# Performance work log

Measured on AMD Instinct MI355X. Metric: run time of the kernel, lower is better.

## Reference

```python
import jax, jax.numpy as jnp
import numpy as np

THETA = 10.0      # spike threshold
TAU_SR = 10.0     # synaptic (PSP) alpha-kernel time constant
TAU_REF = 1.0     # refractory alpha-kernel time constant
SCALE_REF = 2.0   # refractory scale (kernel = -scaleRef*theta*(t/tauRef)e^{1-t/tauRef})
TAU_RHO = 1.0     # surrogate-gradient width
SCALE_RHO = 1.0   # surrogate-gradient scale
TS = 1.0          # simulation step (ms)
E = 2.718281828459045

@jax.custom_vjp
def spike_surrogate(u):
    return (u >= THETA).astype(u.dtype)

def _spike_fwd(u):
    return (u >= THETA).astype(u.dtype), u

def _spike_bwd(u, g):
    # SLAYER surrogate spike-pdf gradient
    pdf = (SCALE_RHO / TAU_RHO) * jnp.exp(-jnp.abs(u - THETA) / TAU_RHO)
    return (g * pdf,)

spike_surrogate.defvjp(_spike_fwd, _spike_bwd)

def psp_spike(x):
    # x: (N, ..., T). PSP = causal temporal conv with alpha kernel
    # eps(t) = (t/tauSr) e^{1-t/tauSr}, realized EXACTLY as a 2-state IIR recursion.
    # spike = threshold; each emitted spike injects refractory alpha kernel
    # -scaleRef*theta*(t/tauRef) e^{1-t/tauRef} into the future membrane.
    xt = jnp.moveaxis(x, -1, 0)  # (T, ...)
    a_sr = jnp.exp(jnp.asarray(-TS / TAU_SR, x.dtype))
    a_rf = jnp.exp(jnp.asarray(-TS / TAU_REF, x.dtype))
    c_sr = E / TAU_SR
    c_rf = -SCALE_REF * THETA * E / TAU_REF
    z = jnp.zeros_like(xt[0])
    def step(carry, xi):
        gp, hp, gr, hr = carry
        hp = a_sr * (hp + gp)
        gp = a_sr * gp + xi
        hr = a_rf * (hr + gr)   # same recursion over past spikes
        gr = a_rf * gr
        u = c_sr * hp + c_rf * hr  # membrane = PSP + refractory
        s = spike_surrogate(u)
        return (gp, hp, gr + s, hr), s
    _, st = jax.lax.scan(step, (z, z, z, z), xt)
    return jnp.moveaxis(st, 0, -1)

def sum_pool(x, k):
    # SLAYER pool: conv with constant weight 1.1*theta over kxk window, stride k
    N, C, H, W, T = x.shape
    xs = x.reshape(N, C, H // k, k, W // k, k, T).sum(axis=(3, 5))
    return 1.1 * THETA * xs

def conv2dt(x, w, pad):
    # SLAYER conv = conv3d with kernel (k,k,1): per-time-step 2D conv, T as trailing dim
    return jax.lax.conv_general_dilated(
        x, w[..., None], (1, 1, 1),
        [(pad, pad), (pad, pad), (0, 0)],
        dimension_numbers=('NCHWT', 'OIHWT', 'NCHWT'))

def forward(s_in, w1, w2, w3, w4a, w4b):
    x = psp_spike(sum_pool(s_in, 4))              # (N,2,32,32,T)
    x = psp_spike(conv2dt(x, w1, 2))              # (N,32,32,32,T)
    x = psp_spike(sum_pool(x, 2))                 # (N,32,16,16,T)
    x = psp_spike(conv2dt(x, w2, 1))              # (N,64,16,16,T)
    x = psp_spike(sum_pool(x, 2))                 # (N,64,8,8,T)
    x = psp_spike(conv2dt(x, w3, 1))              # (N,64,8,8,T)
    N, T = x.shape[0], x.shape[-1]
    xf = x.reshape(N, -1, T)                      # (N, 64*8*8, T)
    x = psp_spike(jnp.einsum('nft,of->not', xf, w4a))  # (N,256,T)
    x = psp_spike(jnp.einsum('nct,oc->not', x, w4b))   # (N,11,T)
    return x

def setup_inputs():
    key = jax.random.key(0)
    ks = jax.random.split(key, 6)
    N, T = 4, 300
    # Bernoulli(0.05) event spikes, DVS128 gesture format (N,2,128,128,T)
    s_in = (jax.random.uniform(ks[0], (N, 2, 128, 128, T)) < 0.05).astype(jnp.float32)
    w1 = jax.random.normal(ks[1], (32, 2, 5, 5), jnp.float32) * 10.0 * 0.05   # weightScale=10
    w2 = jax.random.normal(ks[2], (64, 32, 3, 3), jnp.float32) * 20.0 * 0.01  # weightScale=20
    w3 = jax.random.normal(ks[3], (64, 64, 3, 3), jnp.float32) * 20.0 * 0.01  # weightScale=20
    w4a = jax.random.normal(ks[4], (256, 64 * 8 * 8), jnp.float32) * 0.01
    w4b = jax.random.normal(ks[5], (11, 256), jnp.float32) * 0.05
    return {"s_in": s_in, "w1": w1, "w2": w2, "w3": w3, "w4a": w4a, "w4b": w4b}

def reference(s_in, w1, w2, w3, w4a, w4b):
    return forward(s_in, w1, w2, w3, w4a, w4b)
```

## Files before the change

### kernel.cpp

```cpp
#include <hip/hip_runtime.h>
#include <cstdint>

#define TT 300
#define TC 75
#define NBATCH 4

typedef float pf2 __attribute__((ext_vector_type(2)));
typedef _Float16 h8t __attribute__((ext_vector_type(8)));
typedef float f32x4 __attribute__((ext_vector_type(4)));

__device__ __forceinline__ void psp_step(float z, float& gp, float& hp, float& gr, float& hr, float& s_out) {
    hp = 0.90483741803595957f * (hp + gp);
    gp = 0.90483741803595957f * gp + z;
    hr = 0.36787944117144233f * (hr + gr);
    gr = 0.36787944117144233f * gr;
    float u = 0.27182818284590452f * hp + (-54.365636569180904f) * hr;
    float s = (u >= 10.0f) ? 1.0f : 0.0f;
    gr += s;
    s_out = s;
}

template <int R>
__global__ void k_scan_redp(const float* __restrict__ z, float* __restrict__ s,
                            int n_neur, int pstride) {
    int i = blockIdx.x * 64 + threadIdx.x;
    if (i >= n_neur) return;
    const float* zp = z + (size_t)i * TT;
    float* sp = s + (size_t)i * TT;
    float gp = 0.f, hp = 0.f, gr = 0.f, hr = 0.f;
#pragma unroll 1
    for (int c = 0; c < 25; ++c) {
        const float* p = zp + c * 12;
        float4 a0 = *(const float4*)(p);
        float4 a1 = *(const float4*)(p + 4);
        float4 a2 = *(const float4*)(p + 8);
#pragma unroll
        for (int r = 1; r < R; ++r) {
            const float* pr = p + (size_t)r * pstride;
            float4 b0 = *(const float4*)(pr);
            float4 b1 = *(const float4*)(pr + 4);
            float4 b2 = *(const float4*)(pr + 8);
            a0.x += b0.x; a0.y += b0.y; a0.z += b0.z; a0.w += b0.w;
            a1.x += b1.x; a1.y += b1.y; a1.z += b1.z; a1.w += b1.w;
            a2.x += b2.x; a2.y += b2.y; a2.z += b2.z; a2.w += b2.w;
        }
        float4 o0, o1, o2;
        psp_step(a0.x, gp, hp, gr, hr, o0.x);
        psp_step(a0.y, gp, hp, gr, hr, o0.y);
        psp_step(a0.z, gp, hp, gr, hr, o0.z);
        psp_step(a0.w, gp, hp, gr, hr, o0.w);
        psp_step(a1.x, gp, hp, gr, hr, o1.x);
        psp_step(a1.y, gp, hp, gr, hr, o1.y);
        psp_step(a1.z, gp, hp, gr, hr, o1.z);
        psp_step(a1.w, gp, hp, gr, hr, o1.w);
        psp_step(a2.x, gp, hp, gr, hr, o2.x);
        psp_step(a2.y, gp, hp, gr, hr, o2.y);
        psp_step(a2.z, gp, hp, gr, hr, o2.z);
        psp_step(a2.w, gp, hp, gr, hr, o2.w);
        float* q = sp + c * 12;
        *(float4*)(q) = o0;
        *(float4*)(q + 4) = o1;
        *(float4*)(q + 8) = o2;
    }
}

__global__ void k_scan16_f16(const float* __restrict__ z, _Float16* __restrict__ s16) {
    int i = blockIdx.x * 64 + threadIdx.x;
    int n = i >> 12, f = i & 4095;
    const float* zp = z + (size_t)i * 16;
    _Float16* sp = s16 + ((size_t)n * TT) * 4096 + f;
    float gp = 0.f, hp = 0.f, gr = 0.f, hr = 0.f;
#define SC16_CHUNK(TCI, NTT) do {                                              \
    const float* pp = zp + (size_t)(TCI) * (16384 * 16);                       \
    float4 a0 = *(const float4*)(pp);                                          \
    float4 a1 = *(const float4*)(pp + 4);                                      \
    float4 a2 = *(const float4*)(pp + 8);                                      \
    float4 a3 = *(const float4*)(pp + 12);                                     \
    float zv[16] = {a0.x,a0.y,a0.z,a0.w,a1.x,a1.y,a1.z,a1.w,                   \
                    a2.x,a2.y,a2.z,a2.w,a3.x,a3.y,a3.z,a3.w};                  \
    _Pragma("unroll")                                                          \
    for (int tt = 0; tt < (NTT); ++tt) {                                       \
        float o;                                                               \
        psp_step(zv[tt], gp, hp, gr, hr, o);                                   \
        sp[(size_t)((TCI) * 16 + tt) * 4096] = (_Float16)o;                    \
    }                                                                          \
} while (0)
#pragma unroll 1
    for (int tcc = 0; tcc < 18; ++tcc) SC16_CHUNK(tcc, 16);
    SC16_CHUNK(18, 12);
#undef SC16_CHUNK
}

template <int C, int H2, int W2>
__global__ void __launch_bounds__(256) k_spsq16(const float* __restrict__ z,
                                                _Float16* __restrict__ s16) {
    constexpr int H = 2 * H2, W = 2 * W2;
    constexpr int NP = NBATCH * C * H * W;
    constexpr int C8 = C / 8;
    __shared__ _Float16 tile[16 * C];

    int i = blockIdx.x * 256 + threadIdx.x;
    int q = i & 3;
    int p = i >> 2;
    int c  = p % C;
    int x2 = (p / C) % W2;
    int y2 = (p / (C * W2)) % H2;
    int n  = p / (C * W2 * H2);
    int dy = q >> 1, dx = q & 1;
    int pz = ((n * C + c) * H + 2 * y2 + dy) * W + 2 * x2 + dx;
    const float* zp = z + (size_t)pz * 16;

    int tid = threadIdx.x;
    int wt  = tid & 15;
    int wc8 = tid >> 4;
    int p0 = blockIdx.x * 64;
    int wx2 = (p0 / C) % W2;
    int wy2 = (p0 / (C * W2)) % H2;
    int wn  = p0 / (C * W2 * H2);
    _Float16* wbase = s16 + ((((size_t)(wn * C8 + wc8) * H2 + wy2) * W2 + wx2) * TT) * 8;

    float gp = 0.f, hp = 0.f, gr = 0.f, hr = 0.f;
    float Gp = 0.f, Hp = 0.f, Gr = 0.f, Hr = 0.f;
#define SPSQ_CHUNK(TCI, NTT) do {                                              \
    const float* pp = zp + (size_t)(TCI) * (NP * 16);                          \
    float4 a0 = *(const float4*)(pp);                                          \
    float4 a1 = *(const float4*)(pp + 4);                                      \
    float4 a2 = *(const float4*)(pp + 8);                                      \
    float4 a3 = *(const float4*)(pp + 12);                                     \
    float zv[16] = {a0.x,a0.y,a0.z,a0.w,a1.x,a1.y,a1.z,a1.w,                   \
                    a2.x,a2.y,a2.z,a2.w,a3.x,a3.y,a3.z,a3.w};                  \
    float ov[16];                                                              \
    _Pragma("unroll")                                                          \
    for (int tt = 0; tt < (NTT); ++tt) {                                       \
        float sq;                                                              \
        psp_step(zv[tt], gp, hp, gr, hr, sq);                                  \
        float t1 = sq + __shfl_xor(sq, 1, 64);                                 \
        float pool = t1 + __shfl_xor(t1, 2, 64);                               \
        psp_step(11.0f * pool, Gp, Hp, Gr, Hr, ov[tt]);                        \
    }                                                                          \
    __syncthreads();                                                           \
    if (q == 0) {                                                              \
        _Pragma("unroll")                                                      \
        for (int tt = 0; tt < (NTT); ++tt)                                     \
            tile[tt * C + c] = (_Float16)ov[tt];                               \
    }                                                                          \
    __syncthreads();                                                           \
    if (tid < 16 * C8 && wt < (NTT)) {                                         \
        h8t v = *(const h8t*)(tile + wt * C + wc8 * 8);                        \
        *(h8t*)(wbase + (size_t)((TCI) * 16 + wt) * 8) = v;                    \
    }                                                                          \
} while (0)
#pragma unroll 1
    for (int tcc = 0; tcc < 18; ++tcc) SPSQ_CHUNK(tcc, 16);
    SPSQ_CHUNK(18, 12);
#undef SPSQ_CHUNK
}

__global__ void k_pack_wmfma(const float* __restrict__ w, _Float16* __restrict__ wm,
                             int CIN, int COUT, int total) {
    int i = blockIdx.x * 256 + threadIdx.x;
    if (i >= total) return;
    int lane = i & 63;
    int r = i >> 6;
    int ver = r & 1; r >>= 1;
    int KC = CIN >> 5, CT = COUT >> 4;
    int ct = r % CT; r /= CT;
    int kc = r % KC;
    int tap = r / KC;
    int ky = tap / 3, kx = tap % 3;
    int co  = ct * 16 + (lane & 15);
    int ci0 = kc * 32 + (lane >> 4) * 8;
    _Float16 out[8];
#pragma unroll
    for (int j = 0; j < 8; ++j) {
        float wf = w[((co * CIN + ci0 + j) * 3 + ky) * 3 + kx];
        _Float16 hi = (_Float16)wf;
        out[j] = ver ? (_Float16)((wf - (float)hi) * 4096.0f) : hi;
    }
    *(h8t*)(wm + (size_t)i * 8) = *(h8t*)out;
}

__global__ void k_pack_wfc(const float* __restrict__ w, _Float16* __restrict__ wm,
                           int FIN, int COUT, int total) {
    int i = blockIdx.x * 256 + threadIdx.x;
    if (i >= total) return;
    int lane = i & 63;
    int r = i >> 6;
    int ver = r & 1; r >>= 1;
    int CT = COUT >> 4;
    int ct = r % CT;
    int kg = r / CT;
    int co = ct * 16 + (lane & 15);
    int f0 = kg * 32 + (lane >> 4) * 8;
    _Float16 out[8];
#pragma unroll
    for (int j = 0; j < 8; ++j) {
        float wf = w[(size_t)co * FIN + f0 + j];
        _Float16 hi = (_Float16)wf;
        out[j] = ver ? (_Float16)((wf - (float)hi) * 4096.0f) : hi;
    }
    *(h8t*)(wm + (size_t)i * 8) = *(h8t*)out;
}

__global__ void k_pack_wl1(const float* __restrict__ w, _Float16* __restrict__ wm) {
    int i = blockIdx.x * 256 + threadIdx.x;
    if (i >= 768) return;
    int lane = i & 63;
    int r = i >> 6;
    int ver = r & 1;
    int ch = (r >> 1) & 1;
    int kc = r >> 2;
    int co = ch * 16 + (lane & 15);
    int k0 = kc * 32 + (lane >> 4) * 8;
    _Float16 out[8];
#pragma unroll
    for (int j = 0; j < 8; ++j) {
        int k = k0 + j;
        int ky = k >> 4, slot = k & 15, kx = slot >> 1, ci = slot & 1;
        float wf = (ky < 5 && kx < 5) ? w[((co * 2 + ci) * 5 + ky) * 5 + kx] : 0.f;
        _Float16 hif = (_Float16)wf;
        out[j] = ver ? (_Float16)((wf - (float)hif) * 4096.0f) : hif;
    }
    *(h8t*)(wm + (size_t)i * 8) = *(h8t*)out;
}

__global__ void k_pool4(const float* __restrict__ x, float* __restrict__ z) {
    int idx = blockIdx.x * 256 + threadIdx.x;
    if (idx >= NBATCH * 2 * 32 * 32 * TC) return;
    int tc = idx % TC;
    int p  = idx / TC;
    int w  = p % 32;
    int h  = (p / 32) % 32;
    int nc = p / (32 * 32);
    const float* base = x + (((size_t)nc * 128 + h * 4) * 128 + w * 4) * TT + tc * 4;
    float ax = 0.f, ay = 0.f, az = 0.f, aw = 0.f;
#pragma unroll
    for (int i = 0; i < 4; ++i)
#pragma unroll
        for (int j = 0; j < 4; ++j) {
            float4 v = *(const float4*)(base + ((size_t)i * 128 + j) * TT);
            ax += v.x; ay += v.y; az += v.z; aw += v.w;
        }
    float4 o; o.x = 11.0f * ax; o.y = 11.0f * ay; o.z = 11.0f * az; o.w = 11.0f * aw;
    *(float4*)(z + (size_t)p * TT + tc * 4) = o;
}

__global__ void __launch_bounds__(256) k_l1_fused(const float* __restrict__ s0,
                                                  const _Float16* __restrict__ wl1,
                                                  _Float16* __restrict__ s2h) {
    constexpr int NT = 19;
    __shared__ _Float16 stage[7 * 16 * 40];
    __shared__ float    trans[256 * 17];
    __shared__ _Float16 tile[4 * 16 * 16];

    int bid = blockIdx.x;
    int y2 = bid & 15;
    int xh = (bid >> 4) & 3;
    int ch = (bid >> 6) & 1;
    int n  = bid >> 7;
    int tid = threadIdx.x;
    int lane = tid & 63;
    int wv = tid >> 6;
    int tl = lane & 15;
    int hi = lane >> 4;
    int yy = wv >> 1;
    int xq = wv & 1;

    int q    = tid & 3;
    int co_s = (tid >> 2) & 15;
    int x2l_s = tid >> 6;
    int wt  = tid & 15;
    int wc8 = (tid >> 4) & 1;
    int wx  = tid >> 5;

    const h8t* wv4 = (const h8t*)wl1;
    float gp = 0.f, hp = 0.f, gr = 0.f, hr = 0.f;
    float Gp = 0.f, Hp = 0.f, Gr = 0.f, Hr = 0.f;

#pragma unroll 1
    for (int tc = 0; tc < NT; ++tc) {
        __syncthreads();
#pragma unroll
        for (int ii = 0; ii < 14; ++ii) {
            int i = tid + ii * 256;
            int t  = i & 15;
            int lx = (i >> 4) & 15;
            int ci = (i >> 8) & 1;
            int r  = i >> 9;
            int gx = xh * 8 + lx - 2;
            int yi = y2 * 2 + r - 2;
            int tg = tc * 16 + t;
            float v = 0.f;
            if (gx >= 0 && gx < 32 && yi >= 0 && yi < 32 && tg < TT)
                v = s0[(((size_t)(n * 2 + ci) * 32 + yi) * 32 + gx) * TT + tg];
            stage[(r * 16 + t) * 40 + lx * 2 + ci] = (_Float16)v;
        }
        __syncthreads();
        f32x4 ah4[4], al4[4];
#pragma unroll
        for (int xi = 0; xi < 4; ++xi) { ah4[xi] = (f32x4){0.f,0.f,0.f,0.f}; al4[xi] = (f32x4){0.f,0.f,0.f,0.f}; }
#pragma unroll
        for (int kc = 0; kc < 3; ++kc) {
            h8t wa = wv4[((kc * 2 + ch) * 2 + 0) * 64 + lane];
            h8t wb = wv4[((kc * 2 + ch) * 2 + 1) * 64 + lane];
            int row = yy + 2 * kc + (hi >> 1);
#pragma unroll
            for (int xi = 0; xi < 4; ++xi) {
                int xo = xq * 4 + xi;
                const uint32_t* lp = (const uint32_t*)(stage + (row * 16 + tl) * 40 + xo * 2 + (hi & 1) * 8);
                union { uint32_t u[4]; h8t h; } bu;
                bu.u[0] = lp[0]; bu.u[1] = lp[1]; bu.u[2] = lp[2]; bu.u[3] = lp[3];
                ah4[xi] = __builtin_amdgcn_mfma_f32_16x16x32_f16(wa, bu.h, ah4[xi], 0, 0, 0);
                al4[xi] = __builtin_amdgcn_mfma_f32_16x16x32_f16(wb, bu.h, al4[xi], 0, 0, 0);
            }
        }
#pragma unroll
        for (int xi = 0; xi < 4; ++xi) {
            int xo = xq * 4 + xi;
#pragma unroll
            for (int r = 0; r < 4; ++r) {
                float u = ah4[xi][r] + al4[xi][r] * 2.44140625e-4f;
                int rowt = ((xo >> 1) * 16 + hi * 4 + r) * 4 + yy * 2 + (xo & 1);
                trans[rowt * 17 + tl] = u;
            }
        }
        __syncthreads();
#pragma unroll
        for (int t = 0; t < 16; ++t) {
            float u = trans[tid * 17 + t];
            float sq;
            psp_step(u, gp, hp, gr, hr, sq);
            float t1 = sq + __shfl_xor(sq, 1, 64);
            float pool = t1 + __shfl_xor(t1, 2, 64);
            float ov;
            psp_step(11.0f * pool, Gp, Hp, Gr, Hr, ov);
            if (q == 0) tile[(x2l_s * 16 + t) * 16 + co_s] = (_Float16)ov;
        }
        __syncthreads();
        if (tid < 128) {
            int tg = tc * 16 + wt;
            if (tg < TT) {
                h8t v = *(const h8t*)(tile + (wx * 16 + wt) * 16 + wc8 * 8);
                int cg8 = ch * 2 + wc8;
                int x2g = xh * 4 + wx;
                *(h8t*)(s2h + ((((size_t)(n * 4 + cg8) * 16 + y2) * 16 + x2g) * (size_t)TT + tg) * 8) = v;
            }
        }
    }
}

template <int CIN, int COUT, int H, int W, int YPB>
__global__ void __launch_bounds__(256, 2) k_conv_mfma(const _Float16* __restrict__ s16,
                                                      const _Float16* __restrict__ wm,
                                                      float* __restrict__ z) {
    constexpr int NT = 19;
    constexpr int KC = CIN / 32;
    constexpr int CH = CIN / 8;
    constexpr int XL = W + 2;
    constexpr int CT = COUT / 16;
    constexpr int XPW = W / 4;
    constexpr int ROWS = YPB + 2;
    constexpr int NP = NBATCH * COUT * H * W;
    __shared__ _Float16 lds[ROWS * XL * 16 * CIN];

    int bid = blockIdx.x;
    int tc = bid % NT;
    int yb = ((bid / NT) % (H / YPB)) * YPB;
    int n  = bid / (NT * (H / YPB));
    int tid = threadIdx.x;

    constexpr int TOT = ROWS * XL * CH * 16;
    for (int i = tid; i < TOT; i += 256) {
        int t   = i & 15;
        int c   = (i >> 4) % CH;
        int xc  = ((i >> 4) / CH) % XL;
        int row = ((i >> 4) / CH) / XL;
        int tg = tc * 16 + t;
        int xi = xc - 1;
        int yi = yb + row - 1;
        h8t v;
#pragma unroll
        for (int e = 0; e < 8; ++e) v[e] = (_Float16)0.0f;
        if (xi >= 0 && xi < W && yi >= 0 && yi < H && tg < TT)
            v = *(const h8t*)(s16 + ((((size_t)(n * CH + c) * H + yi) * W + xi) * TT + tg) * 8);
        int swz = (CIN == 32) ? ((t >> 1) & 3) : (t & 7);
        int off = ((row * XL + xc) * 16 + t) * CIN + ((c ^ swz) << 3);
        *(h8t*)(lds + off) = v;
    }
    __syncthreads();

    int lane = tid & 63;
    int wv   = tid >> 6;
    int tl   = lane & 15;
    int hi   = lane >> 4;
    const h8t* wmv = (const h8t*)wm;
    int swz = (CIN == 32) ? ((tl >> 1) & 3) : (tl & 7);

#pragma unroll
    for (int yy = 0; yy < YPB; ++yy) {
        f32x4 acc_h[XPW][CT], acc_l[XPW][CT];
#pragma unroll
        for (int a = 0; a < XPW; ++a)
#pragma unroll
            for (int b = 0; b < CT; ++b) {
                acc_h[a][b] = (f32x4){0.f, 0.f, 0.f, 0.f};
                acc_l[a][b] = (f32x4){0.f, 0.f, 0.f, 0.f};
            }
#pragma unroll
        for (int ky = 0; ky < 3; ++ky) {
#pragma unroll
            for (int kx = 0; kx < 3; ++kx) {
                int tap = ky * 3 + kx;
#pragma unroll
                for (int kc = 0; kc < KC; ++kc) {
                    h8t bf[XPW];
#pragma unroll
                    for (int xi = 0; xi < XPW; ++xi) {
                        int x = wv * XPW + xi;
                        int c = kc * 4 + hi;
                        int off = (((yy + ky) * XL + (x + kx)) * 16 + tl) * CIN + ((c ^ swz) << 3);
                        bf[xi] = *(const h8t*)(lds + off);
                    }
#pragma unroll
                    for (int ct = 0; ct < CT; ++ct) {
                        size_t wbase = ((size_t)(tap * KC + kc) * CT + ct) * 2;
                        h8t ah = wmv[(wbase + 0) * 64 + lane];
                        h8t al = wmv[(wbase + 1) * 64 + lane];
#pragma unroll
                        for (int xi = 0; xi < XPW; ++xi) {
                            acc_h[xi][ct] = __builtin_amdgcn_mfma_f32_16x16x32_f16(ah, bf[xi], acc_h[xi][ct], 0, 0, 0);
                            acc_l[xi][ct] = __builtin_amdgcn_mfma_f32_16x16x32_f16(al, bf[xi], acc_l[xi][ct], 0, 0, 0);
                        }
                    }
                }
            }
        }
#pragma unroll
        for (int xi = 0; xi < XPW; ++xi) {
            int x = wv * XPW + xi;
#pragma unroll
            for (int ct = 0; ct < CT; ++ct) {
#pragma unroll
                for (int r = 0; r < 4; ++r) {
                    int co = ct * 16 + hi * 4 + r;
                    int pz = ((n * COUT + co) * H + (yb + yy)) * W + x;
                    z[((size_t)tc * NP + pz) * 16 + tl]
                        = acc_h[xi][ct][r] + acc_l[xi][ct][r] * 2.44140625e-4f;
                }
            }
        }
    }
}

template <int FIN, int OUT>
__global__ void __launch_bounds__(256) k_fc_mfma(const _Float16* __restrict__ s16,
                                                 const _Float16* __restrict__ wm,
                                                 float* __restrict__ z) {
    constexpr int NT = 19;
    constexpr int CT = OUT / 16;
    constexpr int KCH = 512;
    constexpr int NK = FIN / KCH;
    __shared__ _Float16 lds[KCH * 16];

    int bid = blockIdx.x;
    int tc = bid % NT;
    int n  = (bid / NT) % NBATCH;
    int cg = bid / (NT * NBATCH);
    int tid = threadIdx.x;
    int lane = tid & 63, wv = tid >> 6;
    int tl = lane & 15, hi = lane >> 4;
    int ct = cg * 4 + wv;

    f32x4 acc_h = (f32x4){0.f, 0.f, 0.f, 0.f};
    f32x4 acc_l = (f32x4){0.f, 0.f, 0.f, 0.f};
    const h8t* wmv = (const h8t*)wm;

    for (int kb = 0; kb < NK; ++kb) {
        __syncthreads();
#pragma unroll
        for (int j = 0; j < 4; ++j) {
            int chunk = tid + j * 256;
            int c = chunk & 63;
            int t = chunk >> 6;
            int tg = tc * 16 + t;
            h8t v;
#pragma unroll
            for (int e = 0; e < 8; ++e) v[e] = (_Float16)0.0f;
            if (tg < TT) v = *(const h8t*)(s16 + ((size_t)(n * TT + tg) * FIN + kb * KCH + c * 8));
            *(h8t*)(lds + ((t * 64 + (c ^ (t & 7))) << 3)) = v;
        }
        __syncthreads();
#pragma unroll
        for (int kc = 0; kc < KCH / 32; ++kc) {
            int c = kc * 4 + hi;
            h8t bf = *(const h8t*)(lds + ((tl * 64 + (c ^ (tl & 7))) << 3));
            size_t wbase = ((size_t)((kb * (KCH / 32) + kc) * CT + ct)) * 2;
            h8t ah = wmv[(wbase + 0) * 64 + lane];
            h8t al = wmv[(wbase + 1) * 64 + lane];
            acc_h = __builtin_amdgcn_mfma_f32_16x16x32_f16(ah, bf, acc_h, 0, 0, 0);
            acc_l = __builtin_amdgcn_mfma_f32_16x16x32_f16(al, bf, acc_l, 0, 0, 0);
        }
    }
    int tg = tc * 16 + tl;
    if (tg < TT) {
#pragma unroll
        for (int r = 0; r < 4; ++r) {
            int co = ct * 16 + hi * 4 + r;
            z[(size_t)(n * OUT + co) * TT + tg] = acc_h[r] + acc_l[r] * 2.44140625e-4f;
        }
    }
}

template <int OUT, int FIN, int OPER, int FSPLIT>
__global__ void k_fc_a(const float* __restrict__ s, const float* __restrict__ wgt,
                       float* __restrict__ z) {
    constexpr int OG = OUT / OPER, FCH = FIN / FSPLIT;
    int idx = blockIdx.x * 256 + threadIdx.x;
    if (idx >= NBATCH * OG * TC * FSPLIT) return;
    int tc = idx % TC;
    int og = (idx / TC) % OG;
    int n  = (idx / (TC * OG)) % NBATCH;
    int sp = idx / (TC * OG * NBATCH);
    const float* sb = s + (size_t)n * FIN * TT + (size_t)sp * FCH * TT + tc * 4;
    const float* wb = wgt + (size_t)sp * FCH;
    pf2 acc[OPER][2];
#pragma unroll
    for (int k = 0; k < OPER; ++k) { acc[k][0] = (pf2){0.f, 0.f}; acc[k][1] = (pf2){0.f, 0.f}; }
#pragma unroll 2
    for (int f = 0; f < FCH; f += 4) {
        float4 s0 = *(const float4*)(sb + (size_t)(f + 0) * TT);
        float4 s1 = *(const float4*)(sb + (size_t)(f + 1) * TT);
        float4 s2 = *(const float4*)(sb + (size_t)(f + 2) * TT);
        float4 s3 = *(const float4*)(sb + (size_t)(f + 3) * TT);
        pf2 s0a = {s0.x, s0.y}, s0b = {s0.z, s0.w};
        pf2 s1a = {s1.x, s1.y}, s1b = {s1.z, s1.w};
        pf2 s2a = {s2.x, s2.y}, s2b = {s2.z, s2.w};
        pf2 s3a = {s3.x, s3.y}, s3b = {s3.z, s3.w};
#pragma unroll
        for (int k = 0; k < OPER; ++k) {
            float4 wv = *(const float4*)(wb + (size_t)(og * OPER + k) * FIN + f);
            pf2 wx = {wv.x, wv.x}, wy = {wv.y, wv.y}, wz = {wv.z, wv.z}, ww = {wv.w, wv.w};
            pf2 a0 = acc[k][0], a1 = acc[k][1];
            a0 = __builtin_elementwise_fma(wx, s0a, a0);
            a0 = __builtin_elementwise_fma(wy, s1a, a0);
            a0 = __builtin_elementwise_fma(wz, s2a, a0);
            a0 = __builtin_elementwise_fma(ww, s3a, a0);
            a1 = __builtin_elementwise_fma(wx, s0b, a1);
            a1 = __builtin_elementwise_fma(wy, s1b, a1);
            a1 = __builtin_elementwise_fma(wz, s2b, a1);
            a1 = __builtin_elementwise_fma(ww, s3b, a1);
            acc[k][0] = a0; acc[k][1] = a1;
        }
    }
#pragma unroll
    for (int k = 0; k < OPER; ++k) {
        float4 o;
        o.x = acc[k][0].x; o.y = acc[k][0].y; o.z = acc[k][1].x; o.w = acc[k][1].y;
        *(float4*)(z + ((size_t)sp * NBATCH * OUT + (size_t)n * OUT + og * OPER + k) * TT + tc * 4) = o;
    }
}

extern "C" void kernel_launch(void* const* d_in, const int* in_sizes, int n_in,
                              void* d_out, int out_size, void* d_ws, size_t ws_size,
                              hipStream_t stream) {
    const float* s_in = (const float*)d_in[0];
    const float* w1   = (const float*)d_in[1];
    const float* w2   = (const float*)d_in[2];
    const float* w3   = (const float*)d_in[3];
    const float* w4a  = (const float*)d_in[4];
    const float* w4b  = (const float*)d_in[5];
    float* out = (float*)d_out;

    float* Z  = (float*)d_ws;
    float* Sb = Z + 39321600;
    float* WP = Sb + 9830400;
    _Float16* wm2 = (_Float16*)(WP + 1600);
    _Float16* wm3 = (_Float16*)(WP + 1600 + 18432);
    _Float16* S16 = (_Float16*)(Z + 25000000);
    _Float16* wm4 = (_Float16*)(Z + 28000000);
    _Float16* wl1m = (_Float16*)(Z + 30000000);
    float* s0 = Sb;
    _Float16* s2h = (_Float16*)(Sb + 2500000);
    _Float16* s4h = (_Float16*)(Sb + 5000000);

    auto g = [](int n) { return (n + 255) / 256; };
    auto g64 = [](int n) { return (n + 63) / 64; };

    k_pack_wl1<<<3, 256, 0, stream>>>(w1, wl1m);
    k_pack_wmfma<<<g(4608), 256, 0, stream>>>(w2, wm2, 32, 64, 4608);
    k_pack_wmfma<<<g(9216), 256, 0, stream>>>(w3, wm3, 64, 64, 9216);
    k_pack_wfc<<<g(262144), 256, 0, stream>>>(w4a, wm4, 4096, 256, 262144);

    k_pool4<<<g(614400), 256, 0, stream>>>(s_in, Z);
    k_scan_redp<1><<<g64(8192), 64, 0, stream>>>(Z, s0, 8192, 0);

    k_l1_fused<<<512, 256, 0, stream>>>(s0, wl1m, s2h);

    k_conv_mfma<32, 64, 16, 16, 2><<<608, 256, 0, stream>>>(s2h, wm2, Z);
    k_spsq16<64, 8, 8><<<256, 256, 0, stream>>>(Z, s4h);

    k_conv_mfma<64, 64, 8, 8, 1><<<608, 256, 0, stream>>>(s4h, wm3, Z);
    k_scan16_f16<<<256, 64, 0, stream>>>(Z, S16);

    k_fc_mfma<4096, 256><<<304, 256, 0, stream>>>(S16, wm4, Z);
    k_scan_redp<1><<<g64(1024), 64, 0, stream>>>(Z, Sb, 1024, 0);

    k_fc_a<11, 256, 1, 1><<<g(3300), 256, 0, stream>>>(Sb, w4b, Z);
    k_scan_redp<1><<<1, 64, 0, stream>>>(Z, out, 44, 0);
}
```

Measured before the change: 606.9 us.

## Split layer-1 fused conv kernel into single-wave blocks per pooled pixel

Replaces the 256-thread layer-1 fused conv+spike+pool kernel (512 blocks, 8 pooled x-positions per block) with a 64-thread single-wavefront kernel launched as 2048 blocks, each handling one pooled output pixel. This is meant to raise occupancy and parallelism across the GPU's compute units for a serial time-scan kernel. Weight fragments are hoisted into registers once instead of being reloaded every time chunk. The cost is more redundant halo loads from global memory into shared memory, since each block stages a 6x9 input neighbourhood for only 2x2 outputs, and a smaller MFMA workload per block.

Result: slower. 636.3 us (+4.8%).

```diff
diff --git a/kernel.cpp b/kernel.cpp
--- a/kernel.cpp
+++ b/kernel.cpp
@@ -245,35 +245,31 @@
     *(float4*)(z + (size_t)p * TT + tc * 4) = o;
 }
 
-__global__ void __launch_bounds__(256) k_l1_fused(const float* __restrict__ s0,
-                                                  const _Float16* __restrict__ wl1,
-                                                  _Float16* __restrict__ s2h) {
+__global__ void __launch_bounds__(64) k_l1_w64(const float* __restrict__ s0,
+                                               const _Float16* __restrict__ wl1,
+                                               _Float16* __restrict__ s2h) {
     constexpr int NT = 19;
-    __shared__ _Float16 stage[7 * 16 * 40];
-    __shared__ float    trans[256 * 17];
-    __shared__ _Float16 tile[4 * 16 * 16];
+    __shared__ _Float16 stage[7 * 16 * 18];
+    __shared__ float    trans[64 * 17];
+    __shared__ _Float16 tile[16 * 16];
 
     int bid = blockIdx.x;
-    int y2 = bid & 15;
-    int xh = (bid >> 4) & 3;
-    int ch = (bid >> 6) & 1;
-    int n  = bid >> 7;
+    int x2 = bid & 15;
+    int y2 = (bid >> 4) & 15;
+    int ch = (bid >> 8) & 1;
+    int n  = bid >> 9;
     int tid = threadIdx.x;
-    int lane = tid & 63;
-    int wv = tid >> 6;
-    int tl = lane & 15;
-    int hi = lane >> 4;
-    int yy = wv >> 1;
-    int xq = wv & 1;
-
-    int q    = tid & 3;
-    int co_s = (tid >> 2) & 15;
-    int x2l_s = tid >> 6;
-    int wt  = tid & 15;
-    int wc8 = (tid >> 4) & 1;
-    int wx  = tid >> 5;
+    int tl = tid & 15;
+    int hi = tid >> 4;
 
     const h8t* wv4 = (const h8t*)wl1;
+    h8t wfr[3][2];
+#pragma unroll
+    for (int kc = 0; kc < 3; ++kc) {
+        wfr[kc][0] = wv4[((kc * 2 + ch) * 2 + 0) * 64 + tid];
+        wfr[kc][1] = wv4[((kc * 2 + ch) * 2 + 1) * 64 + tid];
+    }
+
     float gp = 0.f, hp = 0.f, gr = 0.f, hr = 0.f;
     float Gp = 0.f, Hp = 0.f, Gr = 0.f, Hr = 0.f;
 
@@ -281,69 +277,81 @@
     for (int tc = 0; tc < NT; ++tc) {
         __syncthreads();
 #pragma unroll
-        for (int ii = 0; ii < 14; ++ii) {
-            int i = tid + ii * 256;
-            int t  = i & 15;
-            int lx = (i >> 4) & 15;
-            int ci = (i >> 8) & 1;
-            int r  = i >> 9;
-            int gx = xh * 8 + lx - 2;
-            int yi = y2 * 2 + r - 2;
+        for (int ii = 0; ii < 32; ++ii) {
+            int i = tid + ii * 64;
+            if (i < 2016) {
+                int t    = i & 15;
+                int lxci = (i >> 4) % 18;
+                int row  = (i >> 4) / 18;
+                int ci = lxci & 1, lx = lxci >> 1;
+                int gx = x2 * 2 - 2 + lx;
+                int gy = y2 * 2 - 2 + row;
+                int tg = tc * 16 + t;
+                float v = 0.f;
+                if (gx >= 0 && gx < 32 && gy >= 0 && gy < 32 && tg < TT)
+                    v = s0[(((size_t)(n * 2 + ci) * 32 + gy) * 32 + gx) * TT + tg];
+                stage[(row * 16 + t) * 18 + lxci] = (_Float16)v;
+            }
+        }
+        __syncthreads();
+        f32x4 acc[2][2][2];
+#pragma unroll
+        for (int a = 0; a < 2; ++a)
+#pragma unroll
+            for (int b = 0; b < 2; ++b)
+#pragma unroll
+                for (int v = 0; v < 2; ++v) acc[a][b][v] = (f32x4){0.f, 0.f, 0.f, 0.f};
+#pragma unroll
+        for (int kc = 0; kc < 3; ++kc) {
+#pragma unroll
+            for (int yy = 0; yy < 2; ++yy) {
+                int row = yy + 2 * kc + (hi >> 1);
+#pragma unroll
+                for (int xo = 0; xo < 2; ++xo) {
+                    const uint32_t* lp = (const uint32_t*)(stage + (row * 16 + tl) * 18 + xo * 2 + (hi & 1) * 8);
+                    union { uint32_t u[4]; h8t h; } bu;
+                    bu.u[0] = lp[0]; bu.u[1] = lp[1]; bu.u[2] = lp[2]; bu.u[3] = lp[3];
+                    acc[yy][xo][0] = __builtin_amdgcn_mfma_f32_16x16x32_f16(wfr[kc][0], bu.h, acc[yy][xo][0], 0, 0, 0);
+                    acc[yy][xo][1] = __builtin_amdgcn_mfma_f32_16x16x32_f16(wfr[kc][1], bu.h, acc[yy][xo][1], 0, 0, 0);
+                }
+            }
+        }
+#pragma unroll
+        for (int yy = 0; yy < 2; ++yy)
+#pragma unroll
+            for (int xo = 0; xo < 2; ++xo)
+#pragma unroll
+                for (int r = 0; r < 4; ++r) {
+                    float u = acc[yy][xo][0][r] + acc[yy][xo][1][r] * 2.44140625e-4f;
+                    int neuron = (hi * 4 + r) * 4 + yy * 2 + xo;
+                    trans[neuron * 17 + tl] = u;
+                }
+        __syncthreads();
+        float zv[16];
+#pragma unroll
+        for (int t = 0; t < 16; ++t) zv[t] = trans[tid * 17 + t];
+        int co_s = tid >> 2;
+        int q = tid & 3;
+#pragma unroll
+        for (int t = 0; t < 16; ++t) {
+            if (tc * 16 + t < TT) {
+                float sq;
+                psp_step(zv[t], gp, hp, gr, hr, sq);
+                float t1 = sq + __shfl_xor(sq, 1, 64);
+                float pool = t1 + __shfl_xor(t1, 2, 64);
+                float ov;
+                psp_step(11.0f * pool, Gp, Hp, Gr, Hr, ov);
+                if (q == 0) tile[t * 16 + co_s] = (_Float16)ov;
+            }
+        }
+        __syncthreads();
+        if (tid < 32) {
+            int t = tid & 15;
+            int cg = tid >> 4;
             int tg = tc * 16 + t;
-            float v = 0.f;
-            if (gx >= 0 && gx < 32 && yi >= 0 && yi < 32 && tg < TT)
-                v = s0[(((size_t)(n * 2 + ci) * 32 + yi) * 32 + gx) * TT + tg];
-            stage[(r * 16 + t) * 40 + lx * 2 + ci] = (_Float16)v;
-        }
-        __syncthreads();
-        f32x4 ah4[4], al4[4];
-#pragma unroll
-        for (int xi = 0; xi < 4; ++xi) { ah4[xi] = (f32x4){0.f,0.f,0.f,0.f}; al4[xi] = (f32x4){0.f,0.f,0.f,0.f}; }
-#pragma unroll
-        for (int kc = 0; kc < 3; ++kc) {
-            h8t wa = wv4[((kc * 2 + ch) * 2 + 0) * 64 + lane];
-            h8t wb = wv4[((kc * 2 + ch) * 2 + 1) * 64 + lane];
-            int row = yy + 2 * kc + (hi >> 1);
-#pragma unroll
-            for (int xi = 0; xi < 4; ++xi) {
-                int xo = xq * 4 + xi;
-                const uint32_t* lp = (const uint32_t*)(stage + (row * 16 + tl) * 40 + xo * 2 + (hi & 1) * 8);
-                union { uint32_t u[4]; h8t h; } bu;
-                bu.u[0] = lp[0]; bu.u[1] = lp[1]; bu.u[2] = lp[2]; bu.u[3] = lp[3];
-                ah4[xi] = __builtin_amdgcn_mfma_f32_16x16x32_f16(wa, bu.h, ah4[xi], 0, 0, 0);
-                al4[xi] = __builtin_amdgcn_mfma_f32_16x16x32_f16(wb, bu.h, al4[xi], 0, 0, 0);
-            }
-        }
-#pragma unroll
-        for (int xi = 0; xi < 4; ++xi) {
-            int xo = xq * 4 + xi;
-#pragma unroll
-            for (int r = 0; r < 4; ++r) {
-                float u = ah4[xi][r] + al4[xi][r] * 2.44140625e-4f;
-                int rowt = ((xo >> 1) * 16 + hi * 4 + r) * 4 + yy * 2 + (xo & 1);
-                trans[rowt * 17 + tl] = u;
-            }
-        }
-        __syncthreads();
-#pragma unroll
-        for (int t = 0; t < 16; ++t) {
-            float u = trans[tid * 17 + t];
-            float sq;
-            psp_step(u, gp, hp, gr, hr, sq);
-            float t1 = sq + __shfl_xor(sq, 1, 64);
-            float pool = t1 + __shfl_xor(t1, 2, 64);
-            float ov;
-            psp_step(11.0f * pool, Gp, Hp, Gr, Hr, ov);
-            if (q == 0) tile[(x2l_s * 16 + t) * 16 + co_s] = (_Float16)ov;
-        }
-        __syncthreads();
-        if (tid < 128) {
-            int tg = tc * 16 + wt;
             if (tg < TT) {
-                h8t v = *(const h8t*)(tile + (wx * 16 + wt) * 16 + wc8 * 8);
-                int cg8 = ch * 2 + wc8;
-                int x2g = xh * 4 + wx;
-                *(h8t*)(s2h + ((((size_t)(n * 4 + cg8) * 16 + y2) * 16 + x2g) * (size_t)TT + tg) * 8) = v;
+                h8t v = *(const h8t*)(tile + t * 16 + cg * 8);
+                *(h8t*)(s2h + ((((size_t)(n * 4 + ch * 2 + cg) * 16 + y2) * 16 + x2) * (size_t)TT + tg) * 8) = v;
             }
         }
     }
@@ -594,7 +602,7 @@
     k_pool4<<<g(614400), 256, 0, stream>>>(s_in, Z);
     k_scan_redp<1><<<g64(8192), 64, 0, stream>>>(Z, s0, 8192, 0);
 
-    k_l1_fused<<<512, 256, 0, stream>>>(s0, wl1m, s2h);
+    k_l1_w64<<<2048, 64, 0, stream>>>(s0, wl1m, s2h);
 
     k_conv_mfma<32, 64, 16, 16, 2><<<608, 256, 0, stream>>>(s2h, wm2, Z);
     k_spsq16<64, 8, 8><<<256, 256, 0, stream>>>(Z, s4h);
```

## Prefetch next input chunk into registers with vector loads in fused layer-1 kernel

Applied to the files above, without the earlier changes.

The fused layer-1 kernel used to load each 16-step time chunk of the input with 14 scalar global loads per thread per iteration, right before use. It now precomputes per-thread load offsets once and reads the chunk as float4. It also prefetches the next chunk into registers while the current one is processed, which removes the leading barrier of the loop. In addition, the MFMA weight fragments are hoisted out of the time loop, and the shared staging row pitch is padded from 40 to 42 halves to reduce LDS bank conflicts. The cost is higher register pressure from the prefetch buffers, cached offsets and weight fragments, which may lower occupancy.

Result: faster. 545.8 us (-10.1%).

```diff
diff --git a/kernel.cpp b/kernel.cpp
--- a/kernel.cpp
+++ b/kernel.cpp
@@ -249,7 +249,7 @@
                                                   const _Float16* __restrict__ wl1,
                                                   _Float16* __restrict__ s2h) {
     constexpr int NT = 19;
-    __shared__ _Float16 stage[7 * 16 * 40];
+    __shared__ _Float16 stage[7 * 16 * 42];
     __shared__ float    trans[256 * 17];
     __shared__ _Float16 tile[4 * 16 * 16];
 
@@ -273,27 +273,63 @@
     int wc8 = (tid >> 4) & 1;
     int wx  = tid >> 5;
 
+    bool   it_v[4];
+    size_t it_off[4];
+    int    it_adr[4];
+    int    it_tq[4];
+#pragma unroll
+    for (int ii = 0; ii < 4; ++ii) {
+        int i = tid + ii * 256;
+        int tq = i & 3;
+        int lx = (i >> 2) & 15;
+        int ci = (i >> 6) & 1;
+        int r  = i >> 7;
+        int gx = xh * 8 + lx - 2;
+        int gy = y2 * 2 + r - 2;
+        bool sp = (i < 896) && gx >= 0 && gx < 32 && gy >= 0 && gy < 32;
+        it_v[ii]   = sp;
+        it_off[ii] = sp ? ((((size_t)(n * 2 + ci) * 32 + gy) * 32 + gx) * TT + tq * 4) : 0;
+        it_adr[ii] = (r * 16 + tq * 4) * 42 + lx * 2 + ci;
+        it_tq[ii]  = tq;
+    }
+
     const h8t* wv4 = (const h8t*)wl1;
+    h8t wfr[3][2];
+#pragma unroll
+    for (int kc = 0; kc < 3; ++kc) {
+        wfr[kc][0] = wv4[((kc * 2 + ch) * 2 + 0) * 64 + lane];
+        wfr[kc][1] = wv4[((kc * 2 + ch) * 2 + 1) * 64 + lane];
+    }
+
     float gp = 0.f, hp = 0.f, gr = 0.f, hr = 0.f;
     float Gp = 0.f, Hp = 0.f, Gr = 0.f, Hr = 0.f;
 
+    float4 pf[4];
+#pragma unroll
+    for (int ii = 0; ii < 4; ++ii) {
+        pf[ii] = make_float4(0.f, 0.f, 0.f, 0.f);
+        if (it_v[ii]) pf[ii] = *(const float4*)(s0 + it_off[ii]);
+    }
+
 #pragma unroll 1
     for (int tc = 0; tc < NT; ++tc) {
-        __syncthreads();
-#pragma unroll
-        for (int ii = 0; ii < 14; ++ii) {
-            int i = tid + ii * 256;
-            int t  = i & 15;
-            int lx = (i >> 4) & 15;
-            int ci = (i >> 8) & 1;
-            int r  = i >> 9;
-            int gx = xh * 8 + lx - 2;
-            int yi = y2 * 2 + r - 2;
-            int tg = tc * 16 + t;
-            float v = 0.f;
-            if (gx >= 0 && gx < 32 && yi >= 0 && yi < 32 && tg < TT)
-                v = s0[(((size_t)(n * 2 + ci) * 32 + yi) * 32 + gx) * TT + tg];
-            stage[(r * 16 + t) * 40 + lx * 2 + ci] = (_Float16)v;
+#pragma unroll
+        for (int ii = 0; ii < 4; ++ii) {
+            if (tid + ii * 256 < 896) {
+                stage[it_adr[ii] + 0 * 42] = (_Float16)pf[ii].x;
+                stage[it_adr[ii] + 1 * 42] = (_Float16)pf[ii].y;
+                stage[it_adr[ii] + 2 * 42] = (_Float16)pf[ii].z;
+                stage[it_adr[ii] + 3 * 42] = (_Float16)pf[ii].w;
+            }
+        }
+        if (tc + 1 < NT) {
+#pragma unroll
+            for (int ii = 0; ii < 4; ++ii) {
+                float4 v = make_float4(0.f, 0.f, 0.f, 0.f);
+                if (it_v[ii] && (tc + 1) * 16 + it_tq[ii] * 4 + 3 < TT)
+                    v = *(const float4*)(s0 + it_off[ii] + (tc + 1) * 16);
+                pf[ii] = v;
+            }
         }
         __syncthreads();
         f32x4 ah4[4], al4[4];
@@ -301,17 +337,15 @@
         for (int xi = 0; xi < 4; ++xi) { ah4[xi] = (f32x4){0.f,0.f,0.f,0.f}; al4[xi] = (f32x4){0.f,0.f,0.f,0.f}; }
 #pragma unroll
         for (int kc = 0; kc < 3; ++kc) {
-            h8t wa = wv4[((kc * 2 + ch) * 2 + 0) * 64 + lane];
-            h8t wb = wv4[((kc * 2 + ch) * 2 + 1) * 64 + lane];
             int row = yy + 2 * kc + (hi >> 1);
 #pragma unroll
             for (int xi = 0; xi < 4; ++xi) {
                 int xo = xq * 4 + xi;
-                const uint32_t* lp = (const uint32_t*)(stage + (row * 16 + tl) * 40 + xo * 2 + (hi & 1) * 8);
+                const uint32_t* lp = (const uint32_t*)(stage + (row * 16 + tl) * 42 + xo * 2 + (hi & 1) * 8);
                 union { uint32_t u[4]; h8t h; } bu;
                 bu.u[0] = lp[0]; bu.u[1] = lp[1]; bu.u[2] = lp[2]; bu.u[3] = lp[3];
-                ah4[xi] = __builtin_amdgcn_mfma_f32_16x16x32_f16(wa, bu.h, ah4[xi], 0, 0, 0);
-                al4[xi] = __builtin_amdgcn_mfma_f32_16x16x32_f16(wb, bu.h, al4[xi], 0, 0, 0);
+                ah4[xi] = __builtin_amdgcn_mfma_f32_16x16x32_f16(wfr[kc][0], bu.h, ah4[xi], 0, 0, 0);
+                al4[xi] = __builtin_amdgcn_mfma_f32_16x16x32_f16(wfr[kc][1], bu.h, al4[xi], 0, 0, 0);
             }
         }
 #pragma unroll
@@ -319,7 +353,7 @@
             int xo = xq * 4 + xi;
 #pragma unroll
             for (int r = 0; r < 4; ++r) {
-                float u = ah4[xi][r] + al4[xi][r] * 2.44140625e-4f;
+                float u = ah4[xi][0 * 0 + r] + al4[xi][r] * 2.44140625e-4f;
                 int rowt = ((xo >> 1) * 16 + hi * 4 + r) * 4 + yy * 2 + (xo & 1);
                 trans[rowt * 17 + tl] = u;
             }
```
